# Optimization experiments

Measured on AMD Instinct MI355X. Metric: run time of the kernel, lower is better.

Reference implementation:

```python
import jax, jax.numpy as jnp
import numpy as np

EPS = 1e-5

def knn_idx(x, k):
    # x: (B,C,N). Returns (B,N,k) indices of k nearest neighbors (by L2).
    inner = -2.0 * jnp.einsum('bcn,bcm->bnm', x, x)          # (B,N,N)
    xx = jnp.sum(x * x, axis=1)                               # (B,N)
    neg_dist = -xx[:, :, None] - inner - xx[:, None, :]       # (B,N,N)
    _, idx = jax.lax.top_k(neg_dist, k)                       # (B,N,k)
    return idx

def get_graph_features(x, k):
    # x: (B,C,N) -> (B,2C,N,k) with channels = concat(neighbor-center, center)
    B, C, N = x.shape
    idx = knn_idx(x, k)                                       # (B,N,k)
    pts = jnp.transpose(x, (0, 2, 1))                         # (B,N,C)
    nbr = jax.vmap(lambda p, i: p[i])(pts, idx)               # (B,N,k,C)
    ctr = jnp.broadcast_to(pts[:, :, None, :], nbr.shape)     # (B,N,k,C)
    feat = jnp.concatenate([nbr - ctr, ctr], axis=-1)         # (B,N,k,2C)
    return jnp.transpose(feat, (0, 3, 1, 2))                  # (B,2C,N,k)

def conv_bn_relu(y, W, gamma, beta):
    # 1x1 conv (pointwise matmul) + train-mode BatchNorm2d + ReLU
    y = jnp.einsum('oc,bcnk->bonk', W, y)
    mean = jnp.mean(y, axis=(0, 2, 3), keepdims=True)
    var = jnp.var(y, axis=(0, 2, 3), keepdims=True)
    yhat = (y - mean) * jax.lax.rsqrt(var + EPS)
    return jax.nn.relu(yhat * gamma[None, :, None, None] + beta[None, :, None, None])

def setup_inputs() -> dict:
    key = jax.random.key(0)
    ks = jax.random.split(key, 16)
    B, N, k, emb = 8, 2048, 20, 512
    x = jax.random.normal(ks[0], (B, 3, N), dtype=jnp.float32)
    def w(kk, o, c):
        return jax.random.normal(kk, (o, c), dtype=jnp.float32) * (1.0 / np.sqrt(c))
    inp = {
        'x': x, 'k': k,
        'W1': w(ks[1], 64, 6),   'W2': w(ks[2], 64, 64),
        'W3': w(ks[3], 128, 64), 'W4': w(ks[4], 256, 128),
        'W5': w(ks[5], emb, 512),
    }
    for i, c in zip(range(1, 6), [64, 64, 128, 256, emb]):
        inp[f'g{i}'] = 1.0 + 0.1 * jax.random.normal(ks[5 + i], (c,), dtype=jnp.float32)
        inp[f'b{i}'] = 0.1 * jax.random.normal(ks[10 + i], (c,), dtype=jnp.float32)
    return inp

def reference(x, W1, W2, W3, W4, W5, g1, b1, g2, b2, g3, b3, g4, b4, g5, b5, k):
    B, C, N = x.shape
    h = get_graph_features(x, k)                  # (B,6,N,k)
    h = conv_bn_relu(h, W1, g1, b1)               # (B,64,N,k)
    x1 = jnp.max(h, axis=-1, keepdims=True)
    h = conv_bn_relu(h, W2, g2, b2)               # (B,64,N,k)
    x2 = jnp.max(h, axis=-1, keepdims=True)
    h = conv_bn_relu(h, W3, g3, b3)               # (B,128,N,k)
    x3 = jnp.max(h, axis=-1, keepdims=True)
    h = conv_bn_relu(h, W4, g4, b4)               # (B,256,N,k)
    x4 = jnp.max(h, axis=-1, keepdims=True)
    cat = jnp.concatenate([x1, x2, x3, x4], axis=1)  # (B,512,N,1)
    out = conv_bn_relu(cat, W5, g5, b5)              # (B,emb,N,1)
    return out.reshape(B, -1, N)
```

## Files before the change

kernel.cpp:

```cpp
#include <hip/hip_runtime.h>
#include <hip/hip_bf16.h>

typedef __hip_bfloat16 bf16;
typedef __attribute__((ext_vector_type(8))) short short8v;
typedef __attribute__((ext_vector_type(4))) float f32x4;
typedef unsigned int uint;

#define BATCH 8
#define NPTS 2048
#define KNN 20
#define NK (NPTS*KNN)
#define P4 (BATCH*NK)
#define BN_TOT (BATCH*NPTS)

union BU { bf16 h; unsigned short u; };
__device__ __forceinline__ unsigned short f2bf(float f){
    BU bu; bu.h = __float2bfloat16(f); return bu.u;
}
__device__ __forceinline__ float bfu2f(unsigned short u){
    return __uint_as_float(((uint)u) << 16);
}

__global__ void initK(float* __restrict__ shadow, uint* __restrict__ scbiU5)
{
    int t = blockIdx.x*256 + threadIdx.x;
    if (t < 5*16*1024) shadow[t] = 0.f;
    if (t < 512) scbiU5[t] = 0x00003F80u;
}

__global__ void cvtWS(const float* __restrict__ src, short* __restrict__ dst, int Cin)
{
    int t = blockIdx.x*256 + threadIdx.x;
    int co = t / Cin, ci = t - co*Cin;
    dst[(size_t)co*Cin + (ci ^ ((co & 7) << 3))] = (short)f2bf(src[t]);
}

__global__ __launch_bounds__(256)
void knn_kernel(const float* __restrict__ x, int* __restrict__ idx)
{
    #pragma clang fp contract(off)
    __shared__ float sx[3*NPTS];
    __shared__ float sxx[NPTS];
    const int b  = blockIdx.x / (NPTS/4);
    const int nb = blockIdx.x % (NPTS/4);
    const float* xb = x + (size_t)b*3*NPTS;
    for (int i = threadIdx.x; i < 3*NPTS; i += 256) sx[i] = xb[i];
    __syncthreads();
    for (int i = threadIdx.x; i < NPTS; i += 256) {
        float y0 = sx[i], y1 = sx[NPTS+i], y2 = sx[2*NPTS+i];
        sxx[i] = y0*y0 + y1*y1 + y2*y2;
    }
    __syncthreads();

    const int wave = threadIdx.x >> 6;
    const int lane = threadIdx.x & 63;
    const int n = nb*4 + wave;

    const float x0 = sx[n], x1 = sx[NPTS+n], x2 = sx[2*NPTS+n];
    const float xxn = sxx[n];

    constexpr int L = 6;
    float best[L]; int bi[L];
    #pragma unroll
    for (int i = 0; i < L; ++i) { best[i] = -3e38f; bi[i] = 0x7fffffff; }

    #pragma unroll
    for (int j = 0; j < NPTS/64; ++j) {
        int m = lane + j*64;
        float dot = x0*sx[m] + x1*sx[NPTS+m] + x2*sx[2*NPTS+m];
        float v = -xxn - (-2.f*dot) - sxx[m];
        int mi = m;
        #pragma unroll
        for (int i = 0; i < L; ++i) {
            bool sw = v > best[i];
            float tv = sw ? best[i] : v;
            int   ti = sw ? bi[i]   : mi;
            best[i] = sw ? v  : best[i];
            bi[i]   = sw ? mi : bi[i];
            v = tv; mi = ti;
        }
    }

    size_t obase = ((size_t)b*NPTS + n)*KNN;
    int popped = 0;
    #pragma unroll 1
    for (int s = 0; s < KNN; ++s) {
        float mv = best[0]; int mi = bi[0];
        #pragma unroll
        for (int off = 1; off < 64; off <<= 1) {
            float ov = __shfl_xor(mv, off);
            int   oi = __shfl_xor(mi, off);
            if (ov > mv || (ov == mv && oi < mi)) { mv = ov; mi = oi; }
        }
        bool win = (best[0] == mv) && (bi[0] == mi);
        #pragma unroll
        for (int i = 0; i < L-1; ++i) {
            best[i] = win ? best[i+1] : best[i];
            bi[i]   = win ? bi[i+1]   : bi[i];
        }
        best[L-1] = win ? -3e38f     : best[L-1];
        bi[L-1]   = win ? 0x7fffffff : bi[L-1];
        popped += win ? 1 : 0;
        if (lane == 0) idx[obase + s] = mi;
    }

    if (__any(popped >= L)) {
        float B[KNN]; int BI[KNN];
        #pragma unroll
        for (int i = 0; i < KNN; ++i) { B[i] = -3e38f; BI[i] = 0x7fffffff; }
        #pragma unroll 1
        for (int j = 0; j < NPTS/64; ++j) {
            int m = lane + j*64;
            float dot = x0*sx[m] + x1*sx[NPTS+m] + x2*sx[2*NPTS+m];
            float v = -xxn - (-2.f*dot) - sxx[m];
            int mi = m;
            #pragma unroll
            for (int i = 0; i < KNN; ++i) {
                bool sw = v > B[i];
                float tv = sw ? B[i]  : v;
                int   ti = sw ? BI[i] : mi;
                B[i]  = sw ? v  : B[i];
                BI[i] = sw ? mi : BI[i];
                v = tv; mi = ti;
            }
        }
        #pragma unroll 1
        for (int s = 0; s < KNN; ++s) {
            float mv = B[0]; int mi = BI[0];
            #pragma unroll
            for (int off = 1; off < 64; off <<= 1) {
                float ov = __shfl_xor(mv, off);
                int   oi = __shfl_xor(mi, off);
                if (ov > mv || (ov == mv && oi < mi)) { mv = ov; mi = oi; }
            }
            bool win = (B[0] == mv) && (BI[0] == mi);
            #pragma unroll
            for (int i = 0; i < KNN-1; ++i) {
                B[i]  = win ? B[i+1]  : B[i];
                BI[i] = win ? BI[i+1] : BI[i];
            }
            B[KNN-1]  = win ? -3e38f     : B[KNN-1];
            BI[KNN-1] = win ? 0x7fffffff : BI[KNN-1];
            if (lane == 0) idx[obase + s] = mi;
        }
    }
}

__global__ void conv1T(const float* __restrict__ x, const int* __restrict__ idx,
                       const float* __restrict__ W1, bf16* __restrict__ h1)
{
    int p = blockIdx.x*256 + threadIdx.x;
    int b = p / NK;
    int r = p - b*NK;
    int n = r / KNN;
    int j = idx[p];
    const float* xb = x + (size_t)b*3*NPTS;
    float c0 = xb[n], c1 = xb[NPTS+n], c2 = xb[2*NPTS+n];
    float d0 = xb[j]-c0, d1 = xb[NPTS+j]-c1, d2 = xb[2*NPTS+j]-c2;
    uint4* outp = reinterpret_cast<uint4*>(reinterpret_cast<unsigned short*>(h1) + (size_t)p*64);
    #pragma unroll
    for (int ch = 0; ch < 8; ++ch) {
        uint u[4];
        #pragma unroll
        for (int q = 0; q < 4; ++q) {
            const float* wa = W1 + (ch*8 + q*2)*6;
            float a0 = wa[0]*d0 + wa[1]*d1 + wa[2]*d2 + wa[3]*c0 + wa[4]*c1 + wa[5]*c2;
            const float* wb = wa + 6;
            float a1 = wb[0]*d0 + wb[1]*d1 + wb[2]*d2 + wb[3]*c0 + wb[4]*c1 + wb[5]*c2;
            u[q] = (uint)f2bf(a0) | ((uint)f2bf(a1) << 16);
        }
        outp[ch] = make_uint4(u[0], u[1], u[2], u[3]);
    }
}

__global__ void statsT64(const bf16* __restrict__ h, float* __restrict__ shadow)
{
    __shared__ float ls[4][64], lq[4][64];
    int t = threadIdx.x;
    int c = t & 63, grp = t >> 6;
    const unsigned short* hp = reinterpret_cast<const unsigned short*>(h);
    size_t base = (size_t)blockIdx.x*1024;
    float s = 0.f, q = 0.f;
    for (int it = 0; it < 256; ++it) {
        size_t br = base + grp + (size_t)it*4;
        float v = bfu2f(hp[br*64 + c]);
        s += v; q += v*v;
    }
    ls[grp][c] = s; lq[grp][c] = q;
    __syncthreads();
    if (t < 64) {
        float S = ls[0][t]+ls[1][t]+ls[2][t]+ls[3][t];
        float Q = lq[0][t]+lq[1][t]+lq[2][t]+lq[3][t];
        float* sh = shadow + (size_t)(blockIdx.x & 15)*1024;
        atomicAdd(&sh[t], S);
        atomicAdd(&sh[512 + t], Q);
    }
}

__global__ void fin_kernel(const float* __restrict__ shadow,
                           const float* __restrict__ gamma, const float* __restrict__ beta,
                           uint* __restrict__ scbiU, float* __restrict__ scbiF,
                           int C, float invCnt)
{
    for (int c = threadIdx.x; c < C; c += 256) {
        float s = 0.f, q = 0.f;
        #pragma unroll
        for (int i = 0; i < 16; ++i) { s += shadow[i*1024 + c]; q += shadow[i*1024 + 512 + c]; }
        float m = s*invCnt;
        float var = q*invCnt - m*m;
        float rs = rsqrtf(var + 1e-5f);
        float sc = rs * gamma[c];
        float bi = fmaf(-m, sc, beta[c]);
        scbiF[2*c] = sc; scbiF[2*c+1] = bi;
        scbiU[c] = ((uint)f2bf(bi) << 16) | (uint)f2bf(sc);
    }
}

__device__ __forceinline__ short8v actFrag(short8v raw, const uint* se)
{
    short8v a;
    #pragma unroll
    for (int e = 0; e < 8; ++e) {
        float v  = __uint_as_float(((uint)(unsigned short)raw[e]) << 16);
        float sc = __uint_as_float(se[e] << 16);
        float bi = __uint_as_float(se[e] & 0xffff0000u);
        a[e] = (short)f2bf(fmaxf(fmaf(v, sc, bi), 0.f));
    }
    return a;
}

template<int Cout, int Cin, int M, int POOL, int NSPLIT, int KTILE, int BT, int PF>
__global__ __launch_bounds__(BT)
void gemmT(const short* __restrict__ Wb, const bf16* __restrict__ in,
           const uint* __restrict__ scbi, bf16* __restrict__ outT,
           float* __restrict__ shadow, float* __restrict__ pmax, float* __restrict__ pmin)
{
    constexpr int CSPL = Cout/NSPLIT;
    constexpr int NT   = CSPL/16;
    constexpr int ROWS = (BT/64)*16*M;
    constexpr int KSTOT = Cin/32;
    constexpr int KPT   = KTILE/32;
    constexpr int NTILE = Cin/KTILE;
    constexpr size_t WB = (size_t)CSPL*KTILE*2;
    constexpr size_t PB = POOL ? (size_t)ROWS*17*4 : 0;
    constexpr size_t SB = WB > PB ? WB : PB;

    __shared__ __align__(16) char smem[SB];
    short* WsmS = reinterpret_cast<short*>(smem);
    float* poolF = reinterpret_cast<float*>(smem);

    const int tid  = threadIdx.x;
    const int lane = tid & 63;
    const int g = lane >> 4, mr = lane & 15;
    const int wid = tid >> 6;
    const int rowBlk = blockIdx.x*ROWS;
    const int rowW   = rowBlk + wid*(16*M);
    const int ntBase = blockIdx.y*CSPL;
    const short* inS = reinterpret_cast<const short*>(in);

    f32x4 acc[M][NT];
    #pragma unroll
    for (int m = 0; m < M; ++m)
    #pragma unroll
    for (int i = 0; i < NT; ++i) acc[m][i] = (f32x4){0.f,0.f,0.f,0.f};

    short8v araw[M], anext[M];
    if (PF) {
        #pragma unroll
        for (int m = 0; m < M; ++m)
            araw[m] = *reinterpret_cast<const short8v*>(inS + (size_t)(rowW + m*16 + mr)*Cin + 8*g);
    }

    #pragma unroll 1
    for (int kt = 0; kt < NTILE; ++kt) {
        if (kt) __syncthreads();
        {
            const int ktBase = kt*KTILE;
            for (int f8 = tid; f8 < CSPL*KTILE/8; f8 += BT) {
                int f = f8*8;
                int row = f / KTILE, col = f - row*KTILE;
                short8v v = *reinterpret_cast<const short8v*>(
                    Wb + (size_t)(ntBase + row)*Cin + ktBase + col);
                *reinterpret_cast<short8v*>(WsmS + f) = v;
            }
        }
        __syncthreads();

        #pragma unroll
        for (int ksl = 0; ksl < KPT; ++ksl) {
            const int ksg = kt*KPT + ksl;
            const int k0 = ksg*32 + 8*g;
            if (!PF) {
                #pragma unroll
                for (int m = 0; m < M; ++m)
                    araw[m] = *reinterpret_cast<const short8v*>(inS + (size_t)(rowW + m*16 + mr)*Cin + k0);
            } else if (ksg + 1 < KSTOT) {
                #pragma unroll
                for (int m = 0; m < M; ++m)
                    anext[m] = *reinterpret_cast<const short8v*>(inS + (size_t)(rowW + m*16 + mr)*Cin + k0 + 32);
            }
            const uint4* sp = reinterpret_cast<const uint4*>(scbi + k0);
            uint4 s0 = sp[0], s1 = sp[1];
            uint se[8] = {s0.x, s0.y, s0.z, s0.w, s1.x, s1.y, s1.z, s1.w};
            short8v a[M];
            #pragma unroll
            for (int m = 0; m < M; ++m) a[m] = actFrag(araw[m], se);
            const int kx = ksl*32 + 8*g;
            #pragma unroll
            for (int nt = 0; nt < NT; ++nt) {
                const int brow = nt*16 + mr;
                short8v bfr = *reinterpret_cast<const short8v*>(
                    WsmS + brow*KTILE + (kx ^ ((mr & 7) << 3)));
                #pragma unroll
                for (int m = 0; m < M; ++m)
                    acc[m][nt] = __builtin_amdgcn_mfma_f32_16x16x32_bf16(a[m], bfr, acc[m][nt], 0, 0, 0);
            }
            if (PF) {
                #pragma unroll
                for (int m = 0; m < M; ++m) araw[m] = anext[m];
            }
        }
    }

    float* sh = shadow + (size_t)((blockIdx.x ^ blockIdx.y) & 15)*1024;
    #pragma unroll
    for (int nt = 0; nt < NT; ++nt) {
        float s = 0.f, q = 0.f;
        #pragma unroll
        for (int m = 0; m < M; ++m)
        #pragma unroll
        for (int j = 0; j < 4; ++j) { float v = acc[m][nt][j]; s += v; q += v*v; }
        s += __shfl_xor(s, 16); s += __shfl_xor(s, 32);
        q += __shfl_xor(q, 16); q += __shfl_xor(q, 32);
        if (g == 0) {
            atomicAdd(&sh[ntBase + nt*16 + mr], s);
            atomicAdd(&sh[512 + ntBase + nt*16 + mr], q);
        }
    }

    if (!POOL) {
        #pragma unroll
        for (int m = 0; m < M; ++m)
        #pragma unroll
        for (int nt = 0; nt < NT; ++nt)
        #pragma unroll
        for (int j = 0; j < 4; ++j) {
            size_t row = (size_t)rowW + m*16 + g*4 + j;
            outT[row*Cout + ntBase + nt*16 + mr] = __float2bfloat16(acc[m][nt][j]);
        }
    } else {
        __syncthreads();
        #pragma unroll
        for (int nt = 0; nt < NT; ++nt) {
            #pragma unroll
            for (int m = 0; m < M; ++m)
            #pragma unroll
            for (int j = 0; j < 4; ++j) {
                int row = wid*(16*M) + m*16 + g*4 + j;
                poolF[row*17 + mr] = acc[m][nt][j];
            }
            __syncthreads();
            if (tid < (ROWS/KNN)*16) {
                int gg = tid >> 4, cc = tid & 15;
                float mx = -3e38f, mn = 3e38f;
                #pragma unroll
                for (int kk = 0; kk < KNN; ++kk) {
                    float v = poolF[(gg*KNN + kk)*17 + cc];
                    mx = fmaxf(mx, v); mn = fminf(mn, v);
                }
                int grp = rowBlk/KNN + gg;
                int c = ntBase + nt*16 + cc;
                pmax[(size_t)grp*256 + c] = mx;
                pmin[(size_t)grp*256 + c] = mn;
            }
            __syncthreads();
        }
    }
}

template<int C>
__global__ void maxpoolT(const bf16* __restrict__ h, const float* __restrict__ scbiF,
                         bf16* __restrict__ catT, int coff)
{
    constexpr int PB = 256/C;
    int t = threadIdx.x;
    int c = t & (C-1);
    int bn = blockIdx.x*PB + t/C;
    float sc = scbiF[2*c], bi = scbiF[2*c+1];
    const unsigned short* src = reinterpret_cast<const unsigned short*>(h) + (size_t)bn*KNN*C + c;
    float best = -3e38f;
    #pragma unroll
    for (int kk = 0; kk < KNN; ++kk)
        best = fmaxf(best, fmaf(bfu2f(src[kk*C]), sc, bi));
    catT[(size_t)bn*512 + coff + c] = __float2bfloat16(fmaxf(best, 0.f));
}

__global__ void cat4T(const float* __restrict__ pmax, const float* __restrict__ pmin,
                      const float* __restrict__ scbiF, const float* __restrict__ g4,
                      bf16* __restrict__ catT)
{
    int t = blockIdx.x*256 + threadIdx.x;
    int c = t & 255, bn = t >> 8;
    float sc = scbiF[2*c], bi = scbiF[2*c+1];
    float v = (g4[c] >= 0.f) ? pmax[t] : pmin[t];
    catT[(size_t)bn*512 + 256 + c] = __float2bfloat16(fmaxf(fmaf(v, sc, bi), 0.f));
}

__global__ void finalT(const bf16* __restrict__ h5, const float* __restrict__ scbiF,
                       float* __restrict__ out)
{
    __shared__ float ls[64][65];
    int t = threadIdx.x;
    int b = blockIdx.z, n0 = blockIdx.x*64, c0 = blockIdx.y*64;
    int j = t & 63, i0 = t >> 6;
    float sc = scbiF[2*(c0+j)], bi = scbiF[2*(c0+j)+1];
    const unsigned short* hp = reinterpret_cast<const unsigned short*>(h5);
    for (int it = 0; it < 16; ++it) {
        int i = i0 + it*4;
        float v = bfu2f(hp[((size_t)(b*NPTS + n0 + i))*512 + c0 + j]);
        ls[i][j] = fmaxf(fmaf(v, sc, bi), 0.f);
    }
    __syncthreads();
    for (int it = 0; it < 16; ++it) {
        int cr = i0 + it*4;
        out[((size_t)b*512 + c0 + cr)*NPTS + n0 + j] = ls[j][cr];
    }
}

extern "C" void kernel_launch(void* const* d_in, const int* in_sizes, int n_in,
                              void* d_out, int out_size, void* d_ws, size_t ws_size,
                              hipStream_t stream)
{
    const float* x  = (const float*)d_in[0];
    const float* W1 = (const float*)d_in[2];
    const float* W2 = (const float*)d_in[3];
    const float* W3 = (const float*)d_in[4];
    const float* W4 = (const float*)d_in[5];
    const float* W5 = (const float*)d_in[6];
    const float* g1 = (const float*)d_in[7];  const float* b1 = (const float*)d_in[8];
    const float* g2 = (const float*)d_in[9];  const float* b2 = (const float*)d_in[10];
    const float* g3 = (const float*)d_in[11]; const float* b3 = (const float*)d_in[12];
    const float* g4 = (const float*)d_in[13]; const float* b4 = (const float*)d_in[14];
    const float* g5 = (const float*)d_in[15]; const float* b5 = (const float*)d_in[16];
    float* out = (float*)d_out;

    char* w = (char*)d_ws;
    int*   idx    = (int*)w;
    uint*  scbiU  = (uint*)(w + 1310720);
    float* scbiF  = (float*)(w + 1323008);
    float* shadow = (float*)(w + 1343488);
    short* Wb     = (short*)(w + 1671168);
    bf16*  h1     = (bf16*)(w + 2285568);
    float* pmax   = (float*)h1;
    float* pmin   = pmax + (size_t)BN_TOT*256;
    bf16*  h2     = (bf16*)(w + 44228608);
    bf16*  h5     = h2;
    bf16*  h3     = (bf16*)(w + 86171648);
    bf16*  catT   = (bf16*)(w + 170057728);

    short* Wb2 = Wb, *Wb3 = Wb + 4096, *Wb4 = Wb + 12288, *Wb5 = Wb + 45056;
    float* sh1 = shadow, *sh2 = shadow + 16384, *sh3 = shadow + 2*16384,
         * sh4 = shadow + 3*16384, *sh5 = shadow + 4*16384;

    initK<<<320, 256, 0, stream>>>(shadow, scbiU + 5*512);
    cvtWS<<<16,   256, 0, stream>>>(W2, Wb2, 64);
    cvtWS<<<32,   256, 0, stream>>>(W3, Wb3, 64);
    cvtWS<<<128,  256, 0, stream>>>(W4, Wb4, 128);
    cvtWS<<<1024, 256, 0, stream>>>(W5, Wb5, 512);

    knn_kernel<<<BATCH*NPTS/4, 256, 0, stream>>>(x, idx);
    conv1T<<<P4/256, 256, 0, stream>>>(x, idx, W1, h1);

    statsT64<<<320, 256, 0, stream>>>(h1, sh1);
    fin_kernel<<<1, 256, 0, stream>>>(sh1, g1, b1, scbiU, scbiF, 64, 1.f/P4);
    maxpoolT<64><<<BN_TOT/4, 256, 0, stream>>>(h1, scbiF, catT, 0);

    gemmT<64,64,2,0,1,64,256,1><<<dim3(P4/128,1), 256, 0, stream>>>(
        Wb2, h1, scbiU, h2, sh2, nullptr, nullptr);
    fin_kernel<<<1, 256, 0, stream>>>(sh2, g2, b2, scbiU + 512, scbiF + 1024, 64, 1.f/P4);
    maxpoolT<64><<<BN_TOT/4, 256, 0, stream>>>(h2, scbiF + 1024, catT, 64);

    gemmT<128,64,2,0,2,64,256,1><<<dim3(P4/128,2), 256, 0, stream>>>(
        Wb3, h2, scbiU + 512, h3, sh3, nullptr, nullptr);
    fin_kernel<<<1, 256, 0, stream>>>(sh3, g3, b3, scbiU + 1024, scbiF + 2048, 128, 1.f/P4);
    maxpoolT<128><<<BN_TOT/2, 256, 0, stream>>>(h3, scbiF + 2048, catT, 128);

    gemmT<256,128,2,1,2,128,320,1><<<dim3(P4/160,2), 320, 0, stream>>>(
        Wb4, h3, scbiU + 1024, nullptr, sh4, pmax, pmin);
    fin_kernel<<<1, 256, 0, stream>>>(sh4, g4, b4, scbiU + 1536, scbiF + 3072, 256, 1.f/P4);
    cat4T<<<BN_TOT, 256, 0, stream>>>(pmax, pmin, scbiF + 3072, g4, catT);

    gemmT<512,512,2,0,8,128,256,1><<<dim3(BN_TOT/128,8), 256, 0, stream>>>(
        Wb5, catT, scbiU + 5*512, h5, sh5, nullptr, nullptr);
    fin_kernel<<<1, 256, 0, stream>>>(sh5, g5, b5, scbiU + 2048, scbiF + 4096, 512, 1.f/BN_TOT);
    finalT<<<dim3(NPTS/64, 8, BATCH), 256, 0, stream>>>(h5, scbiF + 4096, out);
}
```

Measured before the change: 386.3 us.

## Apply BN+ReLU in maxpool pass and write back, drop activation from GEMM loop

The maxpool kernels now normalise and ReLU the raw bf16 activations, write the activated values back in place, and pool them. This lets the GEMMs consume pre-activated inputs and drop the per-fragment scale/bias unpacking and the bf16 scale/bias table. The pooled epilogue of the layer-4 GEMM now handles two column tiles per barrier using a doubled shared buffer. The cost is an extra full write of each intermediate tensor in maxpool, in exchange for removing ALU work from the MFMA inner loop.

```diff
diff --git a/kernel.cpp b/kernel.cpp
--- a/kernel.cpp
+++ b/kernel.cpp
@@ -21,11 +21,10 @@
     return __uint_as_float(((uint)u) << 16);
 }
 
-__global__ void initK(float* __restrict__ shadow, uint* __restrict__ scbiU5)
+__global__ void initK(float* __restrict__ shadow)
 {
     int t = blockIdx.x*256 + threadIdx.x;
     if (t < 5*16*1024) shadow[t] = 0.f;
-    if (t < 512) scbiU5[t] = 0x00003F80u;
 }
 
 __global__ void cvtWS(const float* __restrict__ src, short* __restrict__ dst, int Cin)
@@ -199,8 +198,7 @@
 
 __global__ void fin_kernel(const float* __restrict__ shadow,
                            const float* __restrict__ gamma, const float* __restrict__ beta,
-                           uint* __restrict__ scbiU, float* __restrict__ scbiF,
-                           int C, float invCnt)
+                           float* __restrict__ scbiF, int C, float invCnt)
 {
     for (int c = threadIdx.x; c < C; c += 256) {
         float s = 0.f, q = 0.f;
@@ -212,28 +210,14 @@
         float sc = rs * gamma[c];
         float bi = fmaf(-m, sc, beta[c]);
         scbiF[2*c] = sc; scbiF[2*c+1] = bi;
-        scbiU[c] = ((uint)f2bf(bi) << 16) | (uint)f2bf(sc);
-    }
-}
-
-__device__ __forceinline__ short8v actFrag(short8v raw, const uint* se)
-{
-    short8v a;
-    #pragma unroll
-    for (int e = 0; e < 8; ++e) {
-        float v  = __uint_as_float(((uint)(unsigned short)raw[e]) << 16);
-        float sc = __uint_as_float(se[e] << 16);
-        float bi = __uint_as_float(se[e] & 0xffff0000u);
-        a[e] = (short)f2bf(fmaxf(fmaf(v, sc, bi), 0.f));
-    }
-    return a;
+    }
 }
 
 template<int Cout, int Cin, int M, int POOL, int NSPLIT, int KTILE, int BT, int PF>
 __global__ __launch_bounds__(BT)
 void gemmT(const short* __restrict__ Wb, const bf16* __restrict__ in,
-           const uint* __restrict__ scbi, bf16* __restrict__ outT,
-           float* __restrict__ shadow, float* __restrict__ pmax, float* __restrict__ pmin)
+           bf16* __restrict__ outT, float* __restrict__ shadow,
+           float* __restrict__ pmax, float* __restrict__ pmin)
 {
     constexpr int CSPL = Cout/NSPLIT;
     constexpr int NT   = CSPL/16;
@@ -242,7 +226,7 @@
     constexpr int KPT   = KTILE/32;
     constexpr int NTILE = Cin/KTILE;
     constexpr size_t WB = (size_t)CSPL*KTILE*2;
-    constexpr size_t PB = POOL ? (size_t)ROWS*17*4 : 0;
+    constexpr size_t PB = POOL ? (size_t)2*ROWS*17*4 : 0;
     constexpr size_t SB = WB > PB ? WB : PB;
 
     __shared__ __align__(16) char smem[SB];
@@ -264,11 +248,11 @@
     #pragma unroll
     for (int i = 0; i < NT; ++i) acc[m][i] = (f32x4){0.f,0.f,0.f,0.f};
 
-    short8v araw[M], anext[M];
+    short8v a[M], anext[M];
     if (PF) {
         #pragma unroll
         for (int m = 0; m < M; ++m)
-            araw[m] = *reinterpret_cast<const short8v*>(inS + (size_t)(rowW + m*16 + mr)*Cin + 8*g);
+            a[m] = *reinterpret_cast<const short8v*>(inS + (size_t)(rowW + m*16 + mr)*Cin + 8*g);
     }
 
     #pragma unroll 1
@@ -293,18 +277,12 @@
             if (!PF) {
                 #pragma unroll
                 for (int m = 0; m < M; ++m)
-                    araw[m] = *reinterpret_cast<const short8v*>(inS + (size_t)(rowW + m*16 + mr)*Cin + k0);
+                    a[m] = *reinterpret_cast<const short8v*>(inS + (size_t)(rowW + m*16 + mr)*Cin + k0);
             } else if (ksg + 1 < KSTOT) {
                 #pragma unroll
                 for (int m = 0; m < M; ++m)
                     anext[m] = *reinterpret_cast<const short8v*>(inS + (size_t)(rowW + m*16 + mr)*Cin + k0 + 32);
             }
-            const uint4* sp = reinterpret_cast<const uint4*>(scbi + k0);
-            uint4 s0 = sp[0], s1 = sp[1];
-            uint se[8] = {s0.x, s0.y, s0.z, s0.w, s1.x, s1.y, s1.z, s1.w};
-            short8v a[M];
-            #pragma unroll
-            for (int m = 0; m < M; ++m) a[m] = actFrag(araw[m], se);
             const int kx = ksl*32 + 8*g;
             #pragma unroll
             for (int nt = 0; nt < NT; ++nt) {
@@ -317,7 +295,7 @@
             }
             if (PF) {
                 #pragma unroll
-                for (int m = 0; m < M; ++m) araw[m] = anext[m];
+                for (int m = 0; m < M; ++m) a[m] = anext[m];
             }
         }
     }
@@ -351,25 +329,30 @@
     } else {
         __syncthreads();
         #pragma unroll
-        for (int nt = 0; nt < NT; ++nt) {
+        for (int np = 0; np < NT/2; ++np) {
             #pragma unroll
-            for (int m = 0; m < M; ++m)
-            #pragma unroll
-            for (int j = 0; j < 4; ++j) {
-                int row = wid*(16*M) + m*16 + g*4 + j;
-                poolF[row*17 + mr] = acc[m][nt][j];
+            for (int hh = 0; hh < 2; ++hh) {
+                #pragma unroll
+                for (int m = 0; m < M; ++m)
+                #pragma unroll
+                for (int j = 0; j < 4; ++j) {
+                    int row = wid*(16*M) + m*16 + g*4 + j;
+                    poolF[hh*(ROWS*17) + row*17 + mr] = acc[m][np*2+hh][j];
+                }
             }
             __syncthreads();
-            if (tid < (ROWS/KNN)*16) {
-                int gg = tid >> 4, cc = tid & 15;
+            if (tid < 2*(ROWS/KNN)*16) {
+                int hh = tid >> 7;
+                int gg = (tid >> 4) & 7;
+                int cc = tid & 15;
                 float mx = -3e38f, mn = 3e38f;
                 #pragma unroll
                 for (int kk = 0; kk < KNN; ++kk) {
-                    float v = poolF[(gg*KNN + kk)*17 + cc];
+                    float v = poolF[hh*(ROWS*17) + (gg*KNN + kk)*17 + cc];
                     mx = fmaxf(mx, v); mn = fminf(mn, v);
                 }
                 int grp = rowBlk/KNN + gg;
-                int c = ntBase + nt*16 + cc;
+                int c = ntBase + (np*2 + hh)*16 + cc;
                 pmax[(size_t)grp*256 + c] = mx;
                 pmin[(size_t)grp*256 + c] = mn;
             }
@@ -379,7 +362,7 @@
 }
 
 template<int C>
-__global__ void maxpoolT(const bf16* __restrict__ h, const float* __restrict__ scbiF,
+__global__ void maxpoolT(bf16* __restrict__ h, const float* __restrict__ scbiF,
                          bf16* __restrict__ catT, int coff)
 {
     constexpr int PB = 256/C;
@@ -387,12 +370,15 @@
     int c = t & (C-1);
     int bn = blockIdx.x*PB + t/C;
     float sc = scbiF[2*c], bi = scbiF[2*c+1];
-    const unsigned short* src = reinterpret_cast<const unsigned short*>(h) + (size_t)bn*KNN*C + c;
-    float best = -3e38f;
-    #pragma unroll
-    for (int kk = 0; kk < KNN; ++kk)
-        best = fmaxf(best, fmaf(bfu2f(src[kk*C]), sc, bi));
-    catT[(size_t)bn*512 + coff + c] = __float2bfloat16(fmaxf(best, 0.f));
+    unsigned short* src = reinterpret_cast<unsigned short*>(h) + (size_t)bn*KNN*C + c;
+    float best = 0.f;
+    #pragma unroll
+    for (int kk = 0; kk < KNN; ++kk) {
+        float a = fmaxf(fmaf(bfu2f(src[kk*C]), sc, bi), 0.f);
+        src[kk*C] = f2bf(a);
+        best = fmaxf(best, a);
+    }
+    catT[(size_t)bn*512 + coff + c] = __float2bfloat16(best);
 }
 
 __global__ void cat4T(const float* __restrict__ pmax, const float* __restrict__ pmin,
@@ -446,7 +432,6 @@
 
     char* w = (char*)d_ws;
     int*   idx    = (int*)w;
-    uint*  scbiU  = (uint*)(w + 1310720);
     float* scbiF  = (float*)(w + 1323008);
     float* shadow = (float*)(w + 1343488);
     short* Wb     = (short*)(w + 1671168);
@@ -462,7 +447,7 @@
     float* sh1 = shadow, *sh2 = shadow + 16384, *sh3 = shadow + 2*16384,
          * sh4 = shadow + 3*16384, *sh5 = shadow + 4*16384;
 
-    initK<<<320, 256, 0, stream>>>(shadow, scbiU + 5*512);
+    initK<<<320, 256, 0, stream>>>(shadow);
     cvtWS<<<16,   256, 0, stream>>>(W2, Wb2, 64);
     cvtWS<<<32,   256, 0, stream>>>(W3, Wb3, 64);
     cvtWS<<<128,  256, 0, stream>>>(W4, Wb4, 128);
@@ -472,26 +457,26 @@
     conv1T<<<P4/256, 256, 0, stream>>>(x, idx, W1, h1);
 
     statsT64<<<320, 256, 0, stream>>>(h1, sh1);
-    fin_kernel<<<1, 256, 0, stream>>>(sh1, g1, b1, scbiU, scbiF, 64, 1.f/P4);
+    fin_kernel<<<1, 256, 0, stream>>>(sh1, g1, b1, scbiF, 64, 1.f/P4);
     maxpoolT<64><<<BN_TOT/4, 256, 0, stream>>>(h1, scbiF, catT, 0);
 
     gemmT<64,64,2,0,1,64,256,1><<<dim3(P4/128,1), 256, 0, stream>>>(
-        Wb2, h1, scbiU, h2, sh2, nullptr, nullptr);
-    fin_kernel<<<1, 256, 0, stream>>>(sh2, g2, b2, scbiU + 512, scbiF + 1024, 64, 1.f/P4);
+        Wb2, h1, h2, sh2, nullptr, nullptr);
+    fin_kernel<<<1, 256, 0, stream>>>(sh2, g2, b2, scbiF + 1024, 64, 1.f/P4);
     maxpoolT<64><<<BN_TOT/4, 256, 0, stream>>>(h2, scbiF + 1024, catT, 64);
 
     gemmT<128,64,2,0,2,64,256,1><<<dim3(P4/128,2), 256, 0, stream>>>(
-        Wb3, h2, scbiU + 512, h3, sh3, nullptr, nullptr);
-    fin_kernel<<<1, 256, 0, stream>>>(sh3, g3, b3, scbiU + 1024, scbiF + 2048, 128, 1.f/P4);
+        Wb3, h2, h3, sh3, nullptr, nullptr);
+    fin_kernel<<<1, 256, 0, stream>>>(sh3, g3, b3, scbiF + 2048, 128, 1.f/P4);
     maxpoolT<128><<<BN_TOT/2, 256, 0, stream>>>(h3, scbiF + 2048, catT, 128);
 
     gemmT<256,128,2,1,2,128,320,1><<<dim3(P4/160,2), 320, 0, stream>>>(
-        Wb4, h3, scbiU + 1024, nullptr, sh4, pmax, pmin);
-    fin_kernel<<<1, 256, 0, stream>>>(sh4, g4, b4, scbiU + 1536, scbiF + 3072, 256, 1.f/P4);
+        Wb4, h3, nullptr, sh4, pmax, pmin);
+    fin_kernel<<<1, 256, 0, stream>>>(sh4, g4, b4, scbiF + 3072, 256, 1.f/P4);
     cat4T<<<BN_TOT, 256, 0, stream>>>(pmax, pmin, scbiF + 3072, g4, catT);
 
     gemmT<512,512,2,0,8,128,256,1><<<dim3(BN_TOT/128,8), 256, 0, stream>>>(
-        Wb5, catT, scbiU + 5*512, h5, sh5, nullptr, nullptr);
-    fin_kernel<<<1, 256, 0, stream>>>(sh5, g5, b5, scbiU + 2048, scbiF + 4096, 512, 1.f/BN_TOT);
+        Wb5, catT, h5, sh5, nullptr, nullptr);
+    fin_kernel<<<1, 256, 0, stream>>>(sh5, g5, b5, scbiF + 4096, 512, 1.f/BN_TOT);
     finalT<<<dim3(NPTS/64, 8, BATCH), 256, 0, stream>>>(h5, scbiF + 4096, out);
 }
```

Result: no change. 392.9 us (+1.7%).
